# Optimization experiments

Hardware: AMD Instinct MI355X
Metric: run time of the kernel (lower is better)

## Reference

```python
import jax, jax.numpy as jnp
import numpy as np

B, N, D = 16, 1024, 768
NEG = -1.0e9

def leaky_relu(x, slope=0.01):
    return jnp.where(x >= 0, x, slope * x)

def setup_inputs() -> dict:
    key = jax.random.key(0)
    ks = jax.random.split(key, 20)
    s = 0.02
    inp = {
        'inputs': jax.random.normal(ks[0], (B, N, D), dtype=jnp.float32),
        'adj_mat': jax.random.randint(ks[1], (B, N, N), 0, 2).astype(jnp.float32),
        # BaseGraphAttNet params
        'W_fc': jax.random.normal(ks[2], (D, D), dtype=jnp.float32) * s,
        'b_fc': jnp.zeros((D,), dtype=jnp.float32),
        'w_q': jax.random.normal(ks[3], (D,), dtype=jnp.float32) * s,
        'b_q': jnp.zeros((), dtype=jnp.float32),
        'w_k': jax.random.normal(ks[4], (D,), dtype=jnp.float32) * s,
        'b_k': jnp.zeros((), dtype=jnp.float32),
        # gating params (6 linears)
        'W_uy': jax.random.normal(ks[5], (D, D), dtype=jnp.float32) * s,
        'b_uy': jnp.zeros((D,), dtype=jnp.float32),
        'W_ux': jax.random.normal(ks[6], (D, D), dtype=jnp.float32) * s,
        'b_ux': jnp.zeros((D,), dtype=jnp.float32),
        'W_ry': jax.random.normal(ks[7], (D, D), dtype=jnp.float32) * s,
        'b_ry': jnp.zeros((D,), dtype=jnp.float32),
        'W_rx': jax.random.normal(ks[8], (D, D), dtype=jnp.float32) * s,
        'b_rx': jnp.zeros((D,), dtype=jnp.float32),
        'W_ty': jax.random.normal(ks[9], (D, D), dtype=jnp.float32) * s,
        'b_ty': jnp.zeros((D,), dtype=jnp.float32),
        'W_tx': jax.random.normal(ks[10], (D, D), dtype=jnp.float32) * s,
        'b_tx': jnp.zeros((D,), dtype=jnp.float32),
    }
    return inp

def reference(inputs, adj_mat, W_fc, b_fc, w_q, b_q, w_k, b_k,
              W_uy, b_uy, W_ux, b_ux, W_ry, b_ry, W_rx, b_rx,
              W_ty, b_ty, W_tx, b_tx):
    # ---- BaseGraphAttNet (residual=False); dropout in eval mode (identity) ----
    feat_proj = jnp.einsum('bnd,ed->bne', inputs, W_fc) + b_fc      # bs x N x D
    q = jnp.einsum('bnd,d->bn', feat_proj, w_q) + b_q               # bs x N
    k = jnp.einsum('bnd,d->bn', feat_proj, w_k) + b_k               # bs x N
    logits = q[:, :, None] + k[:, None, :]                          # bs x N x N
    masked = logits + (1.0 - adj_mat) * NEG
    masked = leaky_relu(masked)
    att = jax.nn.softmax(masked, axis=-1)
    y = jnp.einsum('bnm,bmd->bnd', att, feat_proj)                  # bs x N x D
    # ---- GRU-style gating ----
    u = jax.nn.sigmoid(jnp.einsum('bnd,ed->bne', y, W_uy) + b_uy
                       + jnp.einsum('bnd,ed->bne', inputs, W_ux) + b_ux)
    r = jax.nn.sigmoid(jnp.einsum('bnd,ed->bne', y, W_ry) + b_ry
                       + jnp.einsum('bnd,ed->bne', inputs, W_rx) + b_rx)
    x_tmp = jnp.tanh(jnp.einsum('bnd,ed->bne', y, W_ty) + b_ty
                     + jnp.einsum('bnd,ed->bne', r * inputs, W_tx) + b_tx)
    out = (1.0 - u) * inputs + u * x_tmp
    return out
```

## Files before the change

### kernel.cpp

```cpp
#include <hip/hip_runtime.h>
#include <cmath>

typedef __attribute__((ext_vector_type(8))) short bf16x8;
typedef __attribute__((ext_vector_type(4))) float f32x4;
typedef unsigned short u16;

struct __align__(8) us4 { u16 x, y, z, w; };

__device__ __forceinline__ u16 f2bf(float f) {
    union { float f; unsigned u; } v; v.f = f;
    unsigned u = v.u;
    u += 0x7fffu + ((u >> 16) & 1u);
    return (u16)(u >> 16);
}
__device__ __forceinline__ float bf2f(u16 h) {
    union { unsigned u; float f; } v; v.u = ((unsigned)h) << 16;
    return v.f;
}
__device__ __forceinline__ f32x4 mfma16(bf16x8 a, bf16x8 b, f32x4 c) {
    return __builtin_amdgcn_mfma_f32_16x16x32_bf16(a, b, c, 0, 0, 0);
}
__device__ __forceinline__ void ld_lds16(const u16* g, u16* l) {
    __builtin_amdgcn_global_load_lds(
        (const __attribute__((address_space(1))) unsigned int*)g,
        (__attribute__((address_space(3))) unsigned int*)l, 16, 0, 0);
}

__global__ __launch_bounds__(256) void cvtx(const float* __restrict__ in,
                                            u16* __restrict__ CatA, float* __restrict__ qkz) {
    int i = blockIdx.x * 256 + threadIdx.x;
    float4 f = reinterpret_cast<const float4*>(in)[i];
    us4 o; o.x = f2bf(f.x); o.y = f2bf(f.y); o.z = f2bf(f.z); o.w = f2bf(f.w);
    int row = i / 192, col = (i % 192) * 4;
    *reinterpret_cast<us4*>(CatA + (size_t)row * 1536 + 768 + col) = o;
    if (i < 8192) reinterpret_cast<float4*>(qkz)[i] = float4{0.f, 0.f, 0.f, 0.f};
}

struct WCvt { const float* s[7]; u16* d[7]; int ld[7]; };
__global__ __launch_bounds__(256) void cvtw(WCvt w) {
    int wi = blockIdx.y;
    int i = blockIdx.x * 256 + threadIdx.x;
    float4 f = reinterpret_cast<const float4*>(w.s[wi])[i];
    us4 o; o.x = f2bf(f.x); o.y = f2bf(f.y); o.z = f2bf(f.z); o.w = f2bf(f.w);
    int row = i / 192, col = (i % 192) * 4;
    *reinterpret_cast<us4*>(w.d[wi] + (size_t)row * w.ld[wi] + col) = o;
}

enum { EPI_FPT = 0, EPI_Y, EPI_GATES, EPI_OUT };

struct Epi {
    const float* b1; const float* b2; const float* b3; const float* b4;
    const float* wq; const float* wk; float* qv; float* kv;
    u16* fpT;
    u16* catA;
    const u16* xb;
    u16* ub_o; u16* rxb_o;
    const u16* ub; float* of;
};

template<int EPI, int PH>
__global__ __launch_bounds__(256) void g128(
    const u16* __restrict__ A1, const u16* __restrict__ B1,
    const u16* __restrict__ A2, const u16* __restrict__ B2,
    int K, int ldA1, int ldB1, int ldA2, int ldB2,
    size_t zA, size_t zB, Epi e)
{
    __shared__ u16 lA[128 * 64];
    __shared__ u16 lB[128 * 64];

    const int t = threadIdx.x;
    const int w = t >> 6, lane = t & 63, lm = lane & 15, quad = lane >> 4;
    const int row0 = blockIdx.x * 128;
    int col0, grp = 0;
    if constexpr (EPI == EPI_GATES) { grp = blockIdx.y / 6; col0 = (blockIdx.y % 6) * 128; }
    else col0 = blockIdx.y * 128;

    const int rs2 = t >> 3;
    const int kc2 = (((t & 7) ^ (rs2 & 7)) * 8);
    u16* dA_[4]; u16* dB_[4];
#pragma unroll
    for (int q = 0; q < 4; q++) {
        dA_[q] = lA + q * 2048 + w * 512;
        dB_[q] = lB + q * 2048 + w * 512;
    }

    const int rw0 = (w & 1) * 64, cw0 = (w >> 1) * 64;
    const int ch0 = ((quad) ^ (lm & 7)) * 8;
    const int ch1 = ((quad + 4) ^ (lm & 7)) * 8;
    int laB[4], lbB[4];
#pragma unroll
    for (int i = 0; i < 4; i++) laB[i] = (rw0 + i * 16 + lm) * 64;
#pragma unroll
    for (int j = 0; j < 4; j++) lbB[j] = (cw0 + j * 16 + lm) * 64;

    f32x4 acc[4][4] = {};
    bool first = true;

#pragma unroll
    for (int ph = 0; ph < PH; ph++) {
        const u16* As; const u16* Bs; int ldA, ldB;
        if (ph == 0) { As = A1 + (size_t)blockIdx.z * zA; Bs = B1 + (size_t)blockIdx.z * zB; ldA = ldA1; ldB = ldB1; }
        else         { As = A2; Bs = B2; ldA = ldA2; ldB = ldB2; }
        if constexpr (EPI == EPI_GATES) Bs += (size_t)grp * (768 * 1536);
        const u16* gA = As + (size_t)(row0 + rs2) * ldA + kc2;
        const u16* gB = Bs + (size_t)(col0 + rs2) * ldB + kc2;

        for (int k0 = 0; k0 < K; k0 += 64) {
            if (!first) __syncthreads();
            first = false;
#pragma unroll
            for (int q = 0; q < 4; q++) {
                ld_lds16(gA + (size_t)(q * 32) * ldA + k0, dA_[q]);
                ld_lds16(gB + (size_t)(q * 32) * ldB + k0, dB_[q]);
            }
            __syncthreads();

#pragma unroll
            for (int h = 0; h < 2; h++) {
                const int ch = h ? ch1 : ch0;
                bf16x8 a[4], b[4];
#pragma unroll
                for (int i = 0; i < 4; i++) a[i] = *reinterpret_cast<const bf16x8*>(lA + laB[i] + ch);
#pragma unroll
                for (int j = 0; j < 4; j++) b[j] = *reinterpret_cast<const bf16x8*>(lB + lbB[j] + ch);
#pragma unroll
                for (int i = 0; i < 4; i++)
#pragma unroll
                    for (int j = 0; j < 4; j++)
                        acc[i][j] = mfma16(a[i], b[j], acc[i][j]);
            }
        }
    }

#pragma unroll
    for (int i = 0; i < 4; i++) {
        const int gr = row0 + rw0 + i * 16 + quad * 4;
        if constexpr (EPI == EPI_FPT) {
            float qp[4] = {}, kp[4] = {};
            int bb = gr >> 10, nn = gr & 1023;
#pragma unroll
            for (int j = 0; j < 4; j++) {
                int gc = col0 + cw0 + j * 16 + lm;
                float bias = e.b1[gc];
                float v0 = acc[i][j][0] + bias, v1 = acc[i][j][1] + bias;
                float v2 = acc[i][j][2] + bias, v3 = acc[i][j][3] + bias;
                us4 o; o.x = f2bf(v0); o.y = f2bf(v1); o.z = f2bf(v2); o.w = f2bf(v3);
                *reinterpret_cast<us4*>(e.fpT + (size_t)bb * 786432 + (size_t)gc * 1024 + nn) = o;
                float wqv = e.wq[gc], wkv = e.wk[gc];
                qp[0] = fmaf(v0, wqv, qp[0]); qp[1] = fmaf(v1, wqv, qp[1]);
                qp[2] = fmaf(v2, wqv, qp[2]); qp[3] = fmaf(v3, wqv, qp[3]);
                kp[0] = fmaf(v0, wkv, kp[0]); kp[1] = fmaf(v1, wkv, kp[1]);
                kp[2] = fmaf(v2, wkv, kp[2]); kp[3] = fmaf(v3, wkv, kp[3]);
            }
#pragma unroll
            for (int r = 0; r < 4; r++) {
                float q = qp[r], k = kp[r];
#pragma unroll
                for (int m = 1; m < 16; m <<= 1) { q += __shfl_xor(q, m); k += __shfl_xor(k, m); }
                if (lm == 0) { atomicAdd(e.qv + gr + r, q); atomicAdd(e.kv + gr + r, k); }
            }
        } else if constexpr (EPI == EPI_Y) {
            size_t grow = (size_t)blockIdx.z * 1024 + gr;
#pragma unroll
            for (int j = 0; j < 4; j++) {
                int gc = col0 + cw0 + j * 16 + lm;
#pragma unroll
                for (int r = 0; r < 4; r++)
                    e.catA[(grow + r) * 1536 + gc] = f2bf(acc[i][j][r]);
            }
        } else if constexpr (EPI == EPI_GATES) {
#pragma unroll
            for (int j = 0; j < 4; j++) {
                int gc = col0 + cw0 + j * 16 + lm;
                if (grp == 0) {
                    float bias = e.b1[gc] + e.b2[gc];
#pragma unroll
                    for (int r = 0; r < 4; r++) {
                        size_t idx = (size_t)(gr + r) * 768 + gc;
                        e.ub_o[idx] = f2bf(1.f / (1.f + __expf(-(acc[i][j][r] + bias))));
                    }
                } else {
                    float bias = e.b3[gc] + e.b4[gc];
#pragma unroll
                    for (int r = 0; r < 4; r++) {
                        size_t idx = (size_t)(gr + r) * 768 + gc;
                        float rr = 1.f / (1.f + __expf(-(acc[i][j][r] + bias)));
                        float xv = bf2f(e.xb[(size_t)(gr + r) * 1536 + gc]);
                        e.rxb_o[idx] = f2bf(rr * xv);
                    }
                }
            }
        } else {
#pragma unroll
            for (int j = 0; j < 4; j++) {
                int gc = col0 + cw0 + j * 16 + lm;
                float bias = e.b1[gc] + e.b2[gc];
#pragma unroll
                for (int r = 0; r < 4; r++) {
                    size_t idx = (size_t)(gr + r) * 768 + gc;
                    float tt = tanhf(acc[i][j][r] + bias);
                    float uu = bf2f(e.ub[idx]);
                    float xv = bf2f(e.xb[(size_t)(gr + r) * 1536 + gc]);
                    e.of[idx] = (1.f - uu) * xv + uu * tt;
                }
            }
        }
    }
}

__global__ __launch_bounds__(256) void k_soft4(const float* __restrict__ adj,
                                               const float* __restrict__ qv,
                                               const float* __restrict__ kv,
                                               const float* __restrict__ bq,
                                               const float* __restrict__ bk,
                                               u16* __restrict__ attb) {
    int wv = threadIdx.x >> 6, lane = threadIdx.x & 63;
    int bn = blockIdx.x * 4 + wv;
    int b = bn >> 10;
    const float* adjrow = adj + (size_t)bn * 1024 + lane * 16;
    const float* krow = kv + (b << 10) + lane * 16;
    float q = qv[bn] + bq[0] + bk[0];

    float v[16];
#pragma unroll
    for (int c = 0; c < 4; c++) {
        float4 a4 = *reinterpret_cast<const float4*>(adjrow + c * 4);
        float4 k4 = *reinterpret_cast<const float4*>(krow + c * 4);
        float* vv = v + c * 4;
        vv[0] = q + k4.x + (1.f - a4.x) * -1.0e9f;
        vv[1] = q + k4.y + (1.f - a4.y) * -1.0e9f;
        vv[2] = q + k4.z + (1.f - a4.z) * -1.0e9f;
        vv[3] = q + k4.w + (1.f - a4.w) * -1.0e9f;
    }
#pragma unroll
    for (int t = 0; t < 16; t++) v[t] = v[t] >= 0.f ? v[t] : 0.01f * v[t];

    float mx = v[0];
#pragma unroll
    for (int t = 1; t < 16; t++) mx = fmaxf(mx, v[t]);
#pragma unroll
    for (int off = 32; off; off >>= 1) mx = fmaxf(mx, __shfl_xor(mx, off));

    float s = 0.f;
#pragma unroll
    for (int t = 0; t < 16; t++) { v[t] = __expf(v[t] - mx); s += v[t]; }
#pragma unroll
    for (int off = 32; off; off >>= 1) s += __shfl_xor(s, off);
    float inv = 1.f / s;

    u16* orow = attb + (size_t)bn * 1024 + lane * 16;
#pragma unroll
    for (int c = 0; c < 4; c++) {
        us4 o;
        o.x = f2bf(v[c * 4 + 0] * inv); o.y = f2bf(v[c * 4 + 1] * inv);
        o.z = f2bf(v[c * 4 + 2] * inv); o.w = f2bf(v[c * 4 + 3] * inv);
        *reinterpret_cast<us4*>(orow + c * 4) = o;
    }
}

extern "C" void kernel_launch(void* const* d_in, const int* in_sizes, int n_in,
                              void* d_out, int out_size, void* d_ws, size_t ws_size,
                              hipStream_t stream) {
    const float* x    = (const float*)d_in[0];
    const float* adj  = (const float*)d_in[1];
    const float* W_fc = (const float*)d_in[2];
    const float* b_fc = (const float*)d_in[3];
    const float* w_q  = (const float*)d_in[4];
    const float* b_q  = (const float*)d_in[5];
    const float* w_k  = (const float*)d_in[6];
    const float* b_k  = (const float*)d_in[7];
    const float* W_uy = (const float*)d_in[8];
    const float* b_uy = (const float*)d_in[9];
    const float* W_ux = (const float*)d_in[10];
    const float* b_ux = (const float*)d_in[11];
    const float* W_ry = (const float*)d_in[12];
    const float* b_ry = (const float*)d_in[13];
    const float* W_rx = (const float*)d_in[14];
    const float* b_rx = (const float*)d_in[15];
    const float* W_ty = (const float*)d_in[16];
    const float* b_ty = (const float*)d_in[17];
    const float* W_tx = (const float*)d_in[18];
    const float* b_tx = (const float*)d_in[19];

    char* ws = (char*)d_ws;
    u16*   CatA  = (u16*)  (ws + 0);
    u16*   Wfc_b = (u16*)  (ws + 50331648);
    u16*   Wty_b = (u16*)  (ws + 51511296);
    u16*   Wtx_b = (u16*)  (ws + 52690944);
    u16*   Wg    = (u16*)  (ws + 53870592);
    u16*   fpT   = (u16*)  (ws + 58589184);
    float* qv    = (float*)(ws + 83755008);
    float* kv    = (float*)(ws + 83820544);
    u16*   attb  = (u16*)  (ws + 83886080);
    u16*   u_b   = (u16*)  (ws + 83886080);
    u16*   rxb   = (u16*)  (ws + 117440512);

    cvtx<<<12288, 256, 0, stream>>>(x, CatA, qv);

    WCvt wc;
    wc.s[0] = W_fc; wc.d[0] = Wfc_b;              wc.ld[0] = 768;
    wc.s[1] = W_ty; wc.d[1] = Wty_b;              wc.ld[1] = 768;
    wc.s[2] = W_tx; wc.d[2] = Wtx_b;              wc.ld[2] = 768;
    wc.s[3] = W_uy; wc.d[3] = Wg;                 wc.ld[3] = 1536;
    wc.s[4] = W_ux; wc.d[4] = Wg + 768;           wc.ld[4] = 1536;
    wc.s[5] = W_ry; wc.d[5] = Wg + 768 * 1536;    wc.ld[5] = 1536;
    wc.s[6] = W_rx; wc.d[6] = Wg + 768 * 1536 + 768; wc.ld[6] = 1536;
    cvtw<<<dim3(576, 7), 256, 0, stream>>>(wc);

    Epi e{};
    e = Epi{}; e.b1 = b_fc; e.wq = w_q; e.wk = w_k; e.qv = qv; e.kv = kv; e.fpT = fpT;
    g128<EPI_FPT, 1><<<dim3(128, 6), 256, 0, stream>>>(CatA + 768, Wfc_b, nullptr, nullptr,
                                                       768, 1536, 768, 0, 0, 0, 0, e);

    k_soft4<<<4096, 256, 0, stream>>>(adj, qv, kv, b_q, b_k, attb);

    e = Epi{}; e.catA = CatA;
    g128<EPI_Y, 1><<<dim3(8, 6, 16), 256, 0, stream>>>(attb, fpT, nullptr, nullptr,
                                                       1024, 1024, 1024, 0, 0,
                                                       1048576, 786432, e);
    e = Epi{}; e.b1 = b_uy; e.b2 = b_ux; e.b3 = b_ry; e.b4 = b_rx;
    e.xb = CatA + 768; e.ub_o = u_b; e.rxb_o = rxb;
    g128<EPI_GATES, 1><<<dim3(128, 12), 256, 0, stream>>>(CatA, Wg, nullptr, nullptr,
                                                          1536, 1536, 1536, 0, 0, 0, 0, e);
    e = Epi{}; e.b1 = b_ty; e.b2 = b_tx; e.ub = u_b; e.xb = CatA + 768; e.of = (float*)d_out;
    g128<EPI_OUT, 2><<<dim3(128, 6), 256, 0, stream>>>(CatA, Wty_b, rxb, Wtx_b,
                                                       768, 1536, 768, 768, 768, 0, 0, e);
}
```

Measured before the change: 447.2 us.

## Switch GEMMs to 32x32 MFMA and compute q/k via folded weight vectors

All GEMM tiles now use the 32x32x16 bf16 MFMA instruction with 2x2 accumulators per wave instead of 4x4 16x16 tiles. This cuts LDS reads per MFMA and the instruction count. q and k are now computed algebraically: W_fc^T w_q and W_fc^T w_k are precomputed into folded vectors, and a small kernel takes dot products with x. This removes the atomics and shuffles from the FPT epilogue and the zero-init of q/k. It adds two small launches, and the wprep weight fold is a serial loop of 768 iterations per thread.

```diff
diff --git a/kernel.cpp b/kernel.cpp
--- a/kernel.cpp
+++ b/kernel.cpp
@@ -3,6 +3,7 @@
 
 typedef __attribute__((ext_vector_type(8))) short bf16x8;
 typedef __attribute__((ext_vector_type(4))) float f32x4;
+typedef __attribute__((ext_vector_type(16))) float f32x16;
 typedef unsigned short u16;
 
 struct __align__(8) us4 { u16 x, y, z, w; };
@@ -17,8 +18,8 @@
     union { unsigned u; float f; } v; v.u = ((unsigned)h) << 16;
     return v.f;
 }
-__device__ __forceinline__ f32x4 mfma16(bf16x8 a, bf16x8 b, f32x4 c) {
-    return __builtin_amdgcn_mfma_f32_16x16x32_bf16(a, b, c, 0, 0, 0);
+__device__ __forceinline__ f32x16 mfma32(bf16x8 a, bf16x8 b, f32x16 c) {
+    return __builtin_amdgcn_mfma_f32_32x32x16_bf16(a, b, c, 0, 0, 0);
 }
 __device__ __forceinline__ void ld_lds16(const u16* g, u16* l) {
     __builtin_amdgcn_global_load_lds(
@@ -27,13 +28,12 @@
 }
 
 __global__ __launch_bounds__(256) void cvtx(const float* __restrict__ in,
-                                            u16* __restrict__ CatA, float* __restrict__ qkz) {
+                                            u16* __restrict__ CatA) {
     int i = blockIdx.x * 256 + threadIdx.x;
     float4 f = reinterpret_cast<const float4*>(in)[i];
     us4 o; o.x = f2bf(f.x); o.y = f2bf(f.y); o.z = f2bf(f.z); o.w = f2bf(f.w);
     int row = i / 192, col = (i % 192) * 4;
     *reinterpret_cast<us4*>(CatA + (size_t)row * 1536 + 768 + col) = o;
-    if (i < 8192) reinterpret_cast<float4*>(qkz)[i] = float4{0.f, 0.f, 0.f, 0.f};
 }
 
 struct WCvt { const float* s[7]; u16* d[7]; int ld[7]; };
@@ -46,11 +46,55 @@
     *reinterpret_cast<us4*>(w.d[wi] + (size_t)row * w.ld[wi] + col) = o;
 }
 
+__global__ __launch_bounds__(256) void wprep(const float* __restrict__ Wfc,
+                                             const float* __restrict__ wq,
+                                             const float* __restrict__ wk,
+                                             const float* __restrict__ bfc,
+                                             float* __restrict__ wqp, float* __restrict__ wkp,
+                                             float* __restrict__ qks) {
+    if (blockIdx.x < 3) {
+        int d = blockIdx.x * 256 + threadIdx.x;
+        float sq = 0.f, sk = 0.f;
+        for (int e = 0; e < 768; e++) {
+            float v = Wfc[(size_t)e * 768 + d];
+            sq = fmaf(wq[e], v, sq); sk = fmaf(wk[e], v, sk);
+        }
+        wqp[d] = sq; wkp[d] = sk;
+    } else if (threadIdx.x < 64) {
+        float sq = 0.f, sk = 0.f;
+        for (int e = threadIdx.x; e < 768; e += 64) {
+            sq = fmaf(wq[e], bfc[e], sq); sk = fmaf(wk[e], bfc[e], sk);
+        }
+#pragma unroll
+        for (int off = 32; off; off >>= 1) { sq += __shfl_xor(sq, off); sk += __shfl_xor(sk, off); }
+        if (threadIdx.x == 0) { qks[0] = sq; qks[1] = sk; }
+    }
+}
+
+__global__ __launch_bounds__(256) void k_qk2(const u16* __restrict__ xb,
+                                             const float* __restrict__ wqp,
+                                             const float* __restrict__ wkp,
+                                             const float* __restrict__ qks,
+                                             float* __restrict__ qv, float* __restrict__ kv) {
+    int m = blockIdx.x * 256 + threadIdx.x;
+    const u16* row = xb + (size_t)m * 1536;
+    float sq = 0.f, sk = 0.f;
+    for (int d = 0; d < 768; d += 8) {
+        bf16x8 xv = *reinterpret_cast<const bf16x8*>(row + d);
+#pragma unroll
+        for (int t = 0; t < 8; t++) {
+            float f = bf2f((u16)xv[t]);
+            sq = fmaf(f, wqp[d + t], sq); sk = fmaf(f, wkp[d + t], sk);
+        }
+    }
+    qv[m] = sq + qks[0];
+    kv[m] = sk + qks[1];
+}
+
 enum { EPI_FPT = 0, EPI_Y, EPI_GATES, EPI_OUT };
 
 struct Epi {
     const float* b1; const float* b2; const float* b3; const float* b4;
-    const float* wq; const float* wk; float* qv; float* kv;
     u16* fpT;
     u16* catA;
     const u16* xb;
@@ -69,7 +113,8 @@
     __shared__ u16 lB[128 * 64];
 
     const int t = threadIdx.x;
-    const int w = t >> 6, lane = t & 63, lm = lane & 15, quad = lane >> 4;
+    const int w = t >> 6, lane = t & 63;
+    const int l31 = lane & 31, h = lane >> 5, l7 = lane & 7;
     const int row0 = blockIdx.x * 128;
     int col0, grp = 0;
     if constexpr (EPI == EPI_GATES) { grp = blockIdx.y / 6; col0 = (blockIdx.y % 6) * 128; }
@@ -84,16 +129,21 @@
         dB_[q] = lB + q * 2048 + w * 512;
     }
 
-    const int rw0 = (w & 1) * 64, cw0 = (w >> 1) * 64;
-    const int ch0 = ((quad) ^ (lm & 7)) * 8;
-    const int ch1 = ((quad + 4) ^ (lm & 7)) * 8;
-    int laB[4], lbB[4];
-#pragma unroll
-    for (int i = 0; i < 4; i++) laB[i] = (rw0 + i * 16 + lm) * 64;
-#pragma unroll
-    for (int j = 0; j < 4; j++) lbB[j] = (cw0 + j * 16 + lm) * 64;
-
-    f32x4 acc[4][4] = {};
+    int aof[2][4], bof[2][4];
+#pragma unroll
+    for (int i = 0; i < 2; i++) {
+        int rowA = (w & 1) * 64 + i * 32 + l31;
+#pragma unroll
+        for (int s = 0; s < 4; s++) aof[i][s] = rowA * 64 + (((2 * s + h) ^ l7) * 8);
+    }
+#pragma unroll
+    for (int j = 0; j < 2; j++) {
+        int colB = (w >> 1) * 64 + j * 32 + l31;
+#pragma unroll
+        for (int s = 0; s < 4; s++) bof[j][s] = colB * 64 + (((2 * s + h) ^ l7) * 8);
+    }
+
+    f32x16 acc[2][2] = {};
     bool first = true;
 
 #pragma unroll
@@ -116,93 +166,79 @@
             __syncthreads();
 
 #pragma unroll
-            for (int h = 0; h < 2; h++) {
-                const int ch = h ? ch1 : ch0;
-                bf16x8 a[4], b[4];
-#pragma unroll
-                for (int i = 0; i < 4; i++) a[i] = *reinterpret_cast<const bf16x8*>(lA + laB[i] + ch);
-#pragma unroll
-                for (int j = 0; j < 4; j++) b[j] = *reinterpret_cast<const bf16x8*>(lB + lbB[j] + ch);
-#pragma unroll
-                for (int i = 0; i < 4; i++)
-#pragma unroll
-                    for (int j = 0; j < 4; j++)
-                        acc[i][j] = mfma16(a[i], b[j], acc[i][j]);
+            for (int s = 0; s < 4; s++) {
+                bf16x8 a0 = *reinterpret_cast<const bf16x8*>(lA + aof[0][s]);
+                bf16x8 a1 = *reinterpret_cast<const bf16x8*>(lA + aof[1][s]);
+                bf16x8 b0 = *reinterpret_cast<const bf16x8*>(lB + bof[0][s]);
+                bf16x8 b1 = *reinterpret_cast<const bf16x8*>(lB + bof[1][s]);
+                acc[0][0] = mfma32(a0, b0, acc[0][0]);
+                acc[0][1] = mfma32(a0, b1, acc[0][1]);
+                acc[1][0] = mfma32(a1, b0, acc[1][0]);
+                acc[1][1] = mfma32(a1, b1, acc[1][1]);
             }
         }
     }
 
 #pragma unroll
-    for (int i = 0; i < 4; i++) {
-        const int gr = row0 + rw0 + i * 16 + quad * 4;
-        if constexpr (EPI == EPI_FPT) {
-            float qp[4] = {}, kp[4] = {};
-            int bb = gr >> 10, nn = gr & 1023;
-#pragma unroll
-            for (int j = 0; j < 4; j++) {
-                int gc = col0 + cw0 + j * 16 + lm;
+    for (int i = 0; i < 2; i++) {
+        const int rb = row0 + (w & 1) * 64 + i * 32 + 4 * h;
+#pragma unroll
+        for (int j = 0; j < 2; j++) {
+            const int gc = col0 + (w >> 1) * 64 + j * 32 + l31;
+            if constexpr (EPI == EPI_FPT) {
                 float bias = e.b1[gc];
-                float v0 = acc[i][j][0] + bias, v1 = acc[i][j][1] + bias;
-                float v2 = acc[i][j][2] + bias, v3 = acc[i][j][3] + bias;
-                us4 o; o.x = f2bf(v0); o.y = f2bf(v1); o.z = f2bf(v2); o.w = f2bf(v3);
-                *reinterpret_cast<us4*>(e.fpT + (size_t)bb * 786432 + (size_t)gc * 1024 + nn) = o;
-                float wqv = e.wq[gc], wkv = e.wk[gc];
-                qp[0] = fmaf(v0, wqv, qp[0]); qp[1] = fmaf(v1, wqv, qp[1]);
-                qp[2] = fmaf(v2, wqv, qp[2]); qp[3] = fmaf(v3, wqv, qp[3]);
-                kp[0] = fmaf(v0, wkv, kp[0]); kp[1] = fmaf(v1, wkv, kp[1]);
-                kp[2] = fmaf(v2, wkv, kp[2]); kp[3] = fmaf(v3, wkv, kp[3]);
-            }
-#pragma unroll
-            for (int r = 0; r < 4; r++) {
-                float q = qp[r], k = kp[r];
-#pragma unroll
-                for (int m = 1; m < 16; m <<= 1) { q += __shfl_xor(q, m); k += __shfl_xor(k, m); }
-                if (lm == 0) { atomicAdd(e.qv + gr + r, q); atomicAdd(e.kv + gr + r, k); }
-            }
-        } else if constexpr (EPI == EPI_Y) {
-            size_t grow = (size_t)blockIdx.z * 1024 + gr;
-#pragma unroll
-            for (int j = 0; j < 4; j++) {
-                int gc = col0 + cw0 + j * 16 + lm;
-#pragma unroll
-                for (int r = 0; r < 4; r++)
-                    e.catA[(grow + r) * 1536 + gc] = f2bf(acc[i][j][r]);
-            }
-        } else if constexpr (EPI == EPI_GATES) {
-#pragma unroll
-            for (int j = 0; j < 4; j++) {
-                int gc = col0 + cw0 + j * 16 + lm;
+#pragma unroll
+                for (int g = 0; g < 4; g++) {
+                    int gr0 = rb + 8 * g;
+                    int bb = gr0 >> 10, nn = gr0 & 1023;
+                    us4 o;
+                    o.x = f2bf(acc[i][j][4 * g + 0] + bias);
+                    o.y = f2bf(acc[i][j][4 * g + 1] + bias);
+                    o.z = f2bf(acc[i][j][4 * g + 2] + bias);
+                    o.w = f2bf(acc[i][j][4 * g + 3] + bias);
+                    *reinterpret_cast<us4*>(e.fpT + (size_t)bb * 786432 + (size_t)gc * 1024 + nn) = o;
+                }
+            } else if constexpr (EPI == EPI_Y) {
+                size_t zb = (size_t)blockIdx.z * 1024;
+#pragma unroll
+                for (int g = 0; g < 4; g++)
+#pragma unroll
+                    for (int r = 0; r < 4; r++)
+                        e.catA[(zb + rb + 8 * g + r) * 1536 + gc] = f2bf(acc[i][j][4 * g + r]);
+            } else if constexpr (EPI == EPI_GATES) {
                 if (grp == 0) {
                     float bias = e.b1[gc] + e.b2[gc];
 #pragma unroll
-                    for (int r = 0; r < 4; r++) {
-                        size_t idx = (size_t)(gr + r) * 768 + gc;
-                        e.ub_o[idx] = f2bf(1.f / (1.f + __expf(-(acc[i][j][r] + bias))));
-                    }
+                    for (int g = 0; g < 4; g++)
+#pragma unroll
+                        for (int r = 0; r < 4; r++) {
+                            size_t idx = (size_t)(rb + 8 * g + r) * 768 + gc;
+                            e.ub_o[idx] = f2bf(1.f / (1.f + __expf(-(acc[i][j][4 * g + r] + bias))));
+                        }
                 } else {
                     float bias = e.b3[gc] + e.b4[gc];
 #pragma unroll
+                    for (int g = 0; g < 4; g++)
+#pragma unroll
+                        for (int r = 0; r < 4; r++) {
+                            size_t row = (size_t)(rb + 8 * g + r);
+                            float rr = 1.f / (1.f + __expf(-(acc[i][j][4 * g + r] + bias)));
+                            float xv = bf2f(e.xb[row * 1536 + gc]);
+                            e.rxb_o[row * 768 + gc] = f2bf(rr * xv);
+                        }
+                }
+            } else {
+                float bias = e.b1[gc] + e.b2[gc];
+#pragma unroll
+                for (int g = 0; g < 4; g++)
+#pragma unroll
                     for (int r = 0; r < 4; r++) {
-                        size_t idx = (size_t)(gr + r) * 768 + gc;
-                        float rr = 1.f / (1.f + __expf(-(acc[i][j][r] + bias)));
-                        float xv = bf2f(e.xb[(size_t)(gr + r) * 1536 + gc]);
-                        e.rxb_o[idx] = f2bf(rr * xv);
+                        size_t row = (size_t)(rb + 8 * g + r);
+                        float tt = tanhf(acc[i][j][4 * g + r] + bias);
+                        float uu = bf2f(e.ub[row * 768 + gc]);
+                        float xv = bf2f(e.xb[row * 1536 + gc]);
+                        e.of[row * 768 + gc] = (1.f - uu) * xv + uu * tt;
                     }
-                }
-            }
-        } else {
-#pragma unroll
-            for (int j = 0; j < 4; j++) {
-                int gc = col0 + cw0 + j * 16 + lm;
-                float bias = e.b1[gc] + e.b2[gc];
-#pragma unroll
-                for (int r = 0; r < 4; r++) {
-                    size_t idx = (size_t)(gr + r) * 768 + gc;
-                    float tt = tanhf(acc[i][j][r] + bias);
-                    float uu = bf2f(e.ub[idx]);
-                    float xv = bf2f(e.xb[(size_t)(gr + r) * 1536 + gc]);
-                    e.of[idx] = (1.f - uu) * xv + uu * tt;
-                }
             }
         }
     }
@@ -294,8 +330,11 @@
     u16*   attb  = (u16*)  (ws + 83886080);
     u16*   u_b   = (u16*)  (ws + 83886080);
     u16*   rxb   = (u16*)  (ws + 117440512);
-
-    cvtx<<<12288, 256, 0, stream>>>(x, CatA, qv);
+    float* wqp   = (float*)(ws + 142606336);
+    float* wkp   = (float*)(ws + 142609408);
+    float* qks   = (float*)(ws + 142612480);
+
+    cvtx<<<12288, 256, 0, stream>>>(x, CatA);
 
     WCvt wc;
     wc.s[0] = W_fc; wc.d[0] = Wfc_b;              wc.ld[0] = 768;
@@ -307,13 +346,14 @@
     wc.s[6] = W_rx; wc.d[6] = Wg + 768 * 1536 + 768; wc.ld[6] = 1536;
     cvtw<<<dim3(576, 7), 256, 0, stream>>>(wc);
 
+    wprep<<<4, 256, 0, stream>>>(W_fc, w_q, w_k, b_fc, wqp, wkp, qks);
+    k_qk2<<<64, 256, 0, stream>>>(CatA + 768, wqp, wkp, qks, qv, kv);
+    k_soft4<<<4096, 256, 0, stream>>>(adj, qv, kv, b_q, b_k, attb);
+
     Epi e{};
-    e = Epi{}; e.b1 = b_fc; e.wq = w_q; e.wk = w_k; e.qv = qv; e.kv = kv; e.fpT = fpT;
+    e = Epi{}; e.b1 = b_fc; e.fpT = fpT;
     g128<EPI_FPT, 1><<<dim3(128, 6), 256, 0, stream>>>(CatA + 768, Wfc_b, nullptr, nullptr,
                                                        768, 1536, 768, 0, 0, 0, 0, e);
-
-    k_soft4<<<4096, 256, 0, stream>>>(adj, qv, kv, b_q, b_k, attb);
-
     e = Epi{}; e.catA = CatA;
     g128<EPI_Y, 1><<<dim3(8, 6, 16), 256, 0, stream>>>(attb, fpT, nullptr, nullptr,
                                                        1024, 1024, 1024, 0, 0,
```

Result: slower. 558.7 us (+24.9%).
